# Performance work log

Hardware: AMD Instinct MI355X
Metric: run time of the kernel (lower is better)

Reference implementation:

```python
import jax, jax.numpy as jnp
import numpy as np

EPS = 1e-5

def bn_eval(x, p):
    # p: [4, C] = gamma, beta, running_mean, running_var; channel-last broadcast
    g, b, m, v = p[0], p[1], p[2], p[3]
    return (x - m) * (g / jnp.sqrt(v + EPS)) + b

def _bn_params(k, c):
    k1, k2, k3, k4 = jax.random.split(k, 4)
    gamma = jax.random.uniform(k1, (c,)) + 0.5
    beta = jax.random.normal(k2, (c,)) * 0.1
    mean = jax.random.normal(k3, (c,)) * 0.1
    var = jax.random.uniform(k4, (c,)) + 0.5
    return jnp.stack([gamma, beta, mean, var])

def _lin(k, fan_in, fan_out):
    bound = 1.0 / np.sqrt(fan_in)
    kw, kb = jax.random.split(k)
    w = jax.random.uniform(kw, (fan_in, fan_out), minval=-bound, maxval=bound)
    b = jax.random.uniform(kb, (fan_out,), minval=-bound, maxval=bound)
    return w, b

def setup_inputs() -> dict:
    key = jax.random.key(0)
    B, N, S, C, G = 2, 4096, 16, 256, 8
    ks = jax.random.split(key, 20)
    feats = jax.random.normal(ks[0], (B, N, C), dtype=jnp.float32)
    coords = jax.random.normal(ks[1], (B, N, 3), dtype=jnp.float32)
    index = jax.random.randint(ks[2], (B, N, S), 0, N, dtype=jnp.int32)
    wq, bq = _lin(ks[3], C, C); bnq = _bn_params(ks[4], C)
    wk, bk = _lin(ks[5], C, C); bnk = _bn_params(ks[6], C)
    wv, bv = _lin(ks[7], C, C)
    pm_w1, pm_b1 = _lin(ks[8], 3, C); pm_bn = _bn_params(ks[9], C)
    pm_w2, pm_b2 = _lin(ks[10], C, C)
    pb_w1, pb_b1 = _lin(ks[11], 3, C); pb_bn = _bn_params(ks[12], C)
    pb_w2, pb_b2 = _lin(ks[13], C, C)
    we_w1, we_b1 = _lin(ks[14], C, G); we_bn = _bn_params(ks[15], G)
    we_w2, we_b2 = _lin(ks[16], G, G)
    return dict(feats=feats, coords=coords, index=index,
                wq=wq, bq=bq, bnq=bnq, wk=wk, bk=bk, bnk=bnk, wv=wv, bv=bv,
                pm_w1=pm_w1, pm_b1=pm_b1, pm_bn=pm_bn, pm_w2=pm_w2, pm_b2=pm_b2,
                pb_w1=pb_w1, pb_b1=pb_b1, pb_bn=pb_bn, pb_w2=pb_w2, pb_b2=pb_b2,
                we_w1=we_w1, we_b1=we_b1, we_bn=we_bn, we_w2=we_w2, we_b2=we_b2)

def reference(feats, coords, index,
              wq, bq, bnq, wk, bk, bnk, wv, bv,
              pm_w1, pm_b1, pm_bn, pm_w2, pm_b2,
              pb_w1, pb_b1, pb_bn, pb_w2, pb_b2,
              we_w1, we_b1, we_bn, we_w2, we_b2):
    B, N, C = feats.shape
    S = index.shape[2]
    G = we_w1.shape[1]
    q = jax.nn.relu(bn_eval(feats @ wq + bq, bnq))                       # [B,N,C]
    k = jax.nn.relu(bn_eval(feats @ wk + bk, bnk))                       # [B,N,C]
    v = feats @ wv + bv                                                   # [B,N,C]
    idx = index.reshape(B, N * S)
    key_g = jnp.take_along_axis(k, idx[:, :, None], axis=1).reshape(B, N, S, C)
    val_g = jnp.take_along_axis(v, idx[:, :, None], axis=1).reshape(B, N, S, C)
    crd_g = jnp.take_along_axis(coords, idx[:, :, None], axis=1).reshape(B, N, S, 3)
    relation_qk = key_g - q[:, :, None, :]                                # [B,N,S,C]
    pos = coords[:, :, None, :] - crd_g                                   # [B,N,S,3]
    pem = jax.nn.relu(bn_eval(pos @ pm_w1 + pm_b1, pm_bn)) @ pm_w2 + pm_b2
    relation_qk = relation_qk * pem
    peb = jax.nn.relu(bn_eval(pos @ pb_w1 + pb_b1, pb_bn)) @ pb_w2 + pb_b2
    relation_qk = relation_qk + peb
    val_g = val_g + peb
    w = jax.nn.relu(bn_eval(relation_qk @ we_w1 + we_b1, we_bn)) @ we_w2 + we_b2  # [B,N,S,G]
    w = jax.nn.softmax(w, axis=2)                                         # softmax over neighbors
    val_g = val_g.reshape(B, N, S, G, C // G)
    out = jnp.einsum('bnsgi,bnsg->bngi', val_g, w).reshape(B, N, C)
    return out
```

## Files before the change

kernel.cpp:

```cpp
#include <hip/hip_runtime.h>
#include <hip/hip_bf16.h>


typedef __attribute__((ext_vector_type(8))) short bf16x8_t;
typedef __attribute__((ext_vector_type(4))) float f32x4_t;

#define BN_EPS 1e-5f
#define WSYNC() asm volatile("s_waitcnt lgkmcnt(0)" ::: "memory")

__device__ __forceinline__ float blo(unsigned int v) {
    union { unsigned int u; float f; } x; x.u = v << 16; return x.f;
}
__device__ __forceinline__ float bhi(unsigned int v) {
    union { unsigned int u; float f; } x; x.u = v & 0xffff0000u; return x.f;
}
__device__ __forceinline__ unsigned int fbits(float f) {
    union { float f; unsigned int u; } x; x.f = f; return x.u;
}
__device__ __forceinline__ unsigned short f2b(float f) {
    unsigned int u = fbits(f);
    return (unsigned short)((u + 0x7fffu + ((u >> 16) & 1u)) >> 16);
}
__device__ __forceinline__ unsigned int f2bpk(float a, float b) {
    union { __hip_bfloat162 h; unsigned int u; } x;
    x.h = __float22bfloat162_rn(make_float2(a, b));
    return x.u;
}
__device__ __forceinline__ unsigned int relpair(unsigned int kb, unsigned int qb,
                                                unsigned int pm_, unsigned int pb_) {
    float r0 = (blo(kb) - blo(qb)) * blo(pm_) + blo(pb_);
    float r1 = (bhi(kb) - bhi(qb)) * bhi(pm_) + bhi(pb_);
    return f2bpk(r0, r1);
}

__global__ __launch_bounds__(256) void k_prep(
    const float* __restrict__ wq, const float* __restrict__ wk,
    const float* __restrict__ wv, const float* __restrict__ pm2,
    const float* __restrict__ pb2,
    const float* __restrict__ pm_w1, const float* __restrict__ pm_b1,
    const float* __restrict__ pm_bn,
    const float* __restrict__ pb_w1, const float* __restrict__ pb_b1,
    const float* __restrict__ pb_bn,
    const float* __restrict__ we_w1,
    unsigned short* __restrict__ wsT, float* __restrict__ W4,
    unsigned short* __restrict__ we1TF)
{
    const int bid = blockIdx.x, t = threadIdx.x;
    if (bid < 160) {
        __shared__ unsigned short T[32][72];
        const int mat = bid >> 5;
        const int kk  = (bid >> 2) & 7;
        const int ntq = bid & 3;
        const float* s = (mat == 0) ? wq : (mat == 1) ? wk : (mat == 2) ? wv
                         : (mat == 3) ? pm2 : pb2;
        {
            int c = t & 63, r0 = t >> 6;
            for (int i = 0; i < 8; ++i) {
                int r = r0 + i * 4;
                T[r][c] = f2b(s[(kk * 32 + r) * 256 + ntq * 64 + c]);
            }
        }
        __syncthreads();
        {
            int seg = t >> 6, lane = t & 63;
            int col = seg * 16 + (lane & 15);
            int kr  = (lane >> 4) * 8;
            unsigned int v[8];
            #pragma unroll
            for (int j = 0; j < 8; ++j) v[j] = T[kr + j][col];
            uint4 o;
            o.x = v[0] | (v[1] << 16);
            o.y = v[2] | (v[3] << 16);
            o.z = v[4] | (v[5] << 16);
            o.w = v[6] | (v[7] << 16);
            *(uint4*)(wsT + mat * 65536 + (ntq * 4 + seg) * 4096 + kk * 512 + lane * 8) = o;
        }
    } else if (bid == 160) {
        int c = t;
        float s = pm_bn[c] / sqrtf(pm_bn[768 + c] + BN_EPS);
        float4 wm = make_float4(pm_w1[c] * s, pm_w1[256 + c] * s, pm_w1[512 + c] * s,
                                (pm_b1[c] - pm_bn[512 + c]) * s + pm_bn[256 + c]);
        s = pb_bn[c] / sqrtf(pb_bn[768 + c] + BN_EPS);
        float4 wb = make_float4(pb_w1[c] * s, pb_w1[256 + c] * s, pb_w1[512 + c] * s,
                                (pb_b1[c] - pb_bn[512 + c]) * s + pb_bn[256 + c]);
        ((float4*)W4)[c]       = wm;
        ((float4*)W4)[256 + c] = wb;
    } else {
        for (int j = 0; j < 8; ++j) {
            int e = t * 8 + j;
            int g = e >> 8, c = e & 255;
            we1TF[g * 256 + c] = f2b(we_w1[c * 8 + g]);
        }
    }
}

__global__ __launch_bounds__(256) void k_qkv(
    const float* __restrict__ feats,
    const unsigned short* __restrict__ wT,
    const float* __restrict__ bq, const float* __restrict__ bnq,
    const float* __restrict__ bk, const float* __restrict__ bnk,
    const float* __restrict__ bv,
    unsigned short* __restrict__ qkv)
{
    __shared__ unsigned short A[32][264];
    const int t    = threadIdx.x;
    const int widx = blockIdx.x >> 8;
    const int mb   = blockIdx.x & 255;

    for (int i = 0; i < 8; ++i) {
        int row = 4 * i + (t >> 6), col = (t & 63) * 4;
        float4 f = *(const float4*)(feats + (mb * 32 + row) * 256 + col);
        *(uint2*)&A[row][col] = make_uint2(f2bpk(f.x, f.y), f2bpk(f.z, f.w));
    }
    __syncthreads();

    const int lane = t & 63, w = t >> 6;
    const int ln15 = lane & 15, quad = lane >> 4;
    const int mt = w & 1, nh = w >> 1;

    bf16x8_t afr[8];
    #pragma unroll
    for (int kk = 0; kk < 8; ++kk)
        afr[kk] = *(const bf16x8_t*)&A[mt * 16 + ln15][kk * 32 + quad * 8];

    const unsigned short* W = wT + widx * 65536;
    const float* bias = (widx == 0) ? bq : (widx == 1) ? bk : bv;
    const float* bn   = (widx == 0) ? bnq : (widx == 1) ? bnk : nullptr;
    unsigned short* dst = qkv + (size_t)widx * 8192 * 256;

    const f32x4_t fzero = {0.f, 0.f, 0.f, 0.f};
    f32x4_t acc[8];
    for (int j = 0; j < 8; ++j) acc[j] = fzero;

    #pragma unroll
    for (int kk = 0; kk < 8; ++kk) {
        #pragma unroll
        for (int j = 0; j < 8; ++j) {
            int nt = nh * 8 + j;
            bf16x8_t bfr = *(const bf16x8_t*)(W + ((nt * 8 + kk) * 64 + lane) * 8);
            acc[j] = __builtin_amdgcn_mfma_f32_16x16x32_bf16(afr[kk], bfr, acc[j], 0, 0, 0);
        }
    }

    float bb[8], sc[8], mu[8], be[8];
    #pragma unroll
    for (int j = 0; j < 8; ++j) {
        int c = (nh * 8 + j) * 16 + ln15;
        bb[j] = bias[c];
        if (bn) {
            sc[j] = bn[c] / sqrtf(bn[768 + c] + BN_EPS);
            be[j] = bn[256 + c];
            mu[j] = bn[512 + c];
        }
    }
    __syncthreads();
    #pragma unroll
    for (int j = 0; j < 8; ++j) {
        int c = (nh * 8 + j) * 16 + ln15;
        float y[4];
        for (int r = 0; r < 4; ++r) {
            y[r] = acc[j][r] + bb[j];
            if (bn) y[r] = fmaxf((y[r] - mu[j]) * sc[j] + be[j], 0.f);
        }
        for (int r = 0; r < 4; r += 2) {
            unsigned int pk = f2bpk(y[r], y[r + 1]);
            A[mt * 16 + quad * 4 + r][c]     = (unsigned short)pk;
            A[mt * 16 + quad * 4 + r + 1][c] = (unsigned short)(pk >> 16);
        }
    }
    __syncthreads();
    {
        int row = t >> 3, cc = (t & 7) * 32;
        #pragma unroll
        for (int j = 0; j < 4; ++j) {
            uint4 v = *(const uint4*)&A[row][cc + 8 * j];
            *(uint4*)(dst + (mb * 32 + row) * 256 + cc + 8 * j) = v;
        }
    }
}

__global__ __launch_bounds__(256, 2) void k_main(
    const float* __restrict__ coords,
    const int*   __restrict__ index,
    const unsigned short* __restrict__ qm,
    const unsigned short* __restrict__ km,
    const unsigned short* __restrict__ vm,
    const unsigned short* __restrict__ pmw2F,
    const unsigned short* __restrict__ pbw2F,
    const float* __restrict__ W4,
    const unsigned short* __restrict__ we1TF,
    const float* __restrict__ pm_b2, const float* __restrict__ pb_b2,
    const float* __restrict__ we_b1, const float* __restrict__ we_bn,
    const float* __restrict__ we_w2, const float* __restrict__ we_b2,
    float* __restrict__ out)
{
    __shared__ unsigned short bufR[64][264];
    __shared__ unsigned short bufP[64][264];
    __shared__ float posA[64][4];
    __shared__ float us_[64][8];
    __shared__ int   rowg_[64];
    __shared__ float we2s[8][8];
    __shared__ float web2[8];

    const int t  = threadIdx.x;
    const int P0 = blockIdx.x * 4;
    const int bb_ = P0 >> 12;
    const int w = t >> 6, lane = t & 63;
    const int ln15 = lane & 15, quad = lane >> 4;
    const int R0 = w * 16;
    const int Pg = P0 + w;

    const int rg = (bb_ << 12) + index[Pg * 16 + ln15];
    uint4 kpre[8];
    #pragma unroll
    for (int kk = 0; kk < 8; ++kk)
        kpre[kk] = *(const uint4*)(km + rg * 256 + kk * 32 + quad * 8);

    const int hc = lane * 4;
    float4 cm[4], cb[4];
    #pragma unroll
    for (int i = 0; i < 4; ++i) {
        cm[i] = ((const float4*)W4)[hc + i];
        cb[i] = ((const float4*)W4)[256 + hc + i];
    }
    float bb0[4], bb1[4];
    #pragma unroll
    for (int ntl = 0; ntl < 4; ++ntl) {
        int c = (w * 4 + ntl) * 16 + ln15;
        bb0[ntl] = pb_b2[c];
        bb1[ntl] = pm_b2[c];
    }

    const int g8 = ln15 & 7;
    const float swe_r = we_bn[g8] / sqrtf(we_bn[24 + g8] + BN_EPS);
    const float dwe_r = (we_b1[g8] - we_bn[16 + g8]) * swe_r + we_bn[8 + g8];

    if (lane < 16) {
        rowg_[R0 + lane] = rg;
        posA[R0 + lane][0] = coords[Pg * 3 + 0] - coords[rg * 3 + 0];
        posA[R0 + lane][1] = coords[Pg * 3 + 1] - coords[rg * 3 + 1];
        posA[R0 + lane][2] = coords[Pg * 3 + 2] - coords[rg * 3 + 2];
        posA[R0 + lane][3] = 0.f;
    }
    if (t < 64) we2s[t >> 3][t & 7] = we_w2[t];
    if (t < 8)  web2[t] = we_b2[t];
    WSYNC();

    #pragma unroll
    for (int m = 0; m < 16; ++m) {
        float4 p = *(const float4*)&posA[R0 + m][0];
        float h0 = fmaxf(p.x * cb[0].x + p.y * cb[0].y + p.z * cb[0].z + cb[0].w, 0.f);
        float h1 = fmaxf(p.x * cb[1].x + p.y * cb[1].y + p.z * cb[1].z + cb[1].w, 0.f);
        float h2 = fmaxf(p.x * cb[2].x + p.y * cb[2].y + p.z * cb[2].z + cb[2].w, 0.f);
        float h3 = fmaxf(p.x * cb[3].x + p.y * cb[3].y + p.z * cb[3].z + cb[3].w, 0.f);
        *(uint2*)&bufR[R0 + m][hc] = make_uint2(f2bpk(h0, h1), f2bpk(h2, h3));
    }
    __syncthreads();

    f32x4_t acc[4][4];
    #pragma unroll
    for (int a = 0; a < 4; ++a)
        for (int mt = 0; mt < 4; ++mt)
            acc[a][mt] = (f32x4_t){bb0[a], bb0[a], bb0[a], bb0[a]};
    #pragma unroll
    for (int kk = 0; kk < 8; ++kk) {
        bf16x8_t afr[4];
        #pragma unroll
        for (int mt = 0; mt < 4; ++mt)
            afr[mt] = *(const bf16x8_t*)&bufR[mt * 16 + ln15][kk * 32 + quad * 8];
        #pragma unroll
        for (int ntl = 0; ntl < 4; ++ntl) {
            int nt = w * 4 + ntl;
            bf16x8_t bfr = *(const bf16x8_t*)(pbw2F + ((nt * 8 + kk) * 64 + lane) * 8);
            #pragma unroll
            for (int mt = 0; mt < 4; ++mt)
                acc[ntl][mt] = __builtin_amdgcn_mfma_f32_16x16x32_bf16(afr[mt], bfr, acc[ntl][mt], 0, 0, 0);
        }
    }
    __syncthreads();

    #pragma unroll
    for (int ntl = 0; ntl < 4; ++ntl) {
        int c = (w * 4 + ntl) * 16 + ln15;
        for (int mt = 0; mt < 4; ++mt)
            for (int r = 0; r < 4; r += 2) {
                unsigned int pk = f2bpk(acc[ntl][mt][r], acc[ntl][mt][r + 1]);
                bufP[mt * 16 + quad * 4 + r][c]     = (unsigned short)pk;
                bufP[mt * 16 + quad * 4 + r + 1][c] = (unsigned short)(pk >> 16);
            }
    }
    #pragma unroll
    for (int m = 0; m < 16; ++m) {
        float4 p = *(const float4*)&posA[R0 + m][0];
        float h0 = fmaxf(p.x * cm[0].x + p.y * cm[0].y + p.z * cm[0].z + cm[0].w, 0.f);
        float h1 = fmaxf(p.x * cm[1].x + p.y * cm[1].y + p.z * cm[1].z + cm[1].w, 0.f);
        float h2 = fmaxf(p.x * cm[2].x + p.y * cm[2].y + p.z * cm[2].z + cm[2].w, 0.f);
        float h3 = fmaxf(p.x * cm[3].x + p.y * cm[3].y + p.z * cm[3].z + cm[3].w, 0.f);
        *(uint2*)&bufR[R0 + m][hc] = make_uint2(f2bpk(h0, h1), f2bpk(h2, h3));
    }
    __syncthreads();

    #pragma unroll
    for (int a = 0; a < 4; ++a)
        for (int mt = 0; mt < 4; ++mt)
            acc[a][mt] = (f32x4_t){bb1[a], bb1[a], bb1[a], bb1[a]};
    #pragma unroll
    for (int kk = 0; kk < 8; ++kk) {
        bf16x8_t afr[4];
        #pragma unroll
        for (int mt = 0; mt < 4; ++mt)
            afr[mt] = *(const bf16x8_t*)&bufR[mt * 16 + ln15][kk * 32 + quad * 8];
        #pragma unroll
        for (int ntl = 0; ntl < 4; ++ntl) {
            int nt = w * 4 + ntl;
            bf16x8_t bfr = *(const bf16x8_t*)(pmw2F + ((nt * 8 + kk) * 64 + lane) * 8);
            #pragma unroll
            for (int mt = 0; mt < 4; ++mt)
                acc[ntl][mt] = __builtin_amdgcn_mfma_f32_16x16x32_bf16(afr[mt], bfr, acc[ntl][mt], 0, 0, 0);
        }
    }
    __syncthreads();

    #pragma unroll
    for (int ntl = 0; ntl < 4; ++ntl) {
        int c = (w * 4 + ntl) * 16 + ln15;
        for (int mt = 0; mt < 4; ++mt)
            for (int r = 0; r < 4; r += 2) {
                unsigned int pk = f2bpk(acc[ntl][mt][r], acc[ntl][mt][r + 1]);
                bufR[mt * 16 + quad * 4 + r][c]     = (unsigned short)pk;
                bufR[mt * 16 + quad * 4 + r + 1][c] = (unsigned short)(pk >> 16);
            }
    }
    __syncthreads();

    {
        const bf16x8_t bz = {0, 0, 0, 0, 0, 0, 0, 0};
        f32x4_t lacc = {0.f, 0.f, 0.f, 0.f};
        #pragma unroll
        for (int kk = 0; kk < 8; ++kk) {
            int cb8 = kk * 32 + quad * 8;
            uint4 pm4 = *(const uint4*)&bufR[R0 + ln15][cb8];
            uint4 pb4 = *(const uint4*)&bufP[R0 + ln15][cb8];
            uint4 q4  = *(const uint4*)(qm + Pg * 256 + cb8);
            union { uint4 u; bf16x8_t v; } rr;
            rr.u.x = relpair(kpre[kk].x, q4.x, pm4.x, pb4.x);
            rr.u.y = relpair(kpre[kk].y, q4.y, pm4.y, pb4.y);
            rr.u.z = relpair(kpre[kk].z, q4.z, pm4.z, pb4.z);
            rr.u.w = relpair(kpre[kk].w, q4.w, pm4.w, pb4.w);
            bf16x8_t bfr = bz;
            if (ln15 < 8) bfr = *(const bf16x8_t*)(we1TF + ln15 * 256 + cb8);
            lacc = __builtin_amdgcn_mfma_f32_16x16x32_bf16(rr.v, bfr, lacc, 0, 0, 0);
        }
        if (ln15 < 8) {
            #pragma unroll
            for (int r = 0; r < 4; ++r)
                us_[R0 + quad * 4 + r][ln15] = fmaxf(lacc[r] * swe_r + dwe_r, 0.f);
        }
    }
    WSYNC();

    if (lane < 16) {
        float uv[8], l[8];
        #pragma unroll
        for (int gp = 0; gp < 8; ++gp) uv[gp] = us_[R0 + lane][gp];
        #pragma unroll
        for (int g = 0; g < 8; ++g) {
            float x = web2[g];
            for (int gp = 0; gp < 8; ++gp) x += uv[gp] * we2s[gp][g];
            l[g] = x;
        }
        #pragma unroll
        for (int g = 0; g < 8; ++g) us_[R0 + lane][g] = l[g];
    }
    WSYNC();

    if (lane < 8) {
        int g = lane;
        float mx = -1e30f;
        for (int s = 0; s < 16; ++s) mx = fmaxf(mx, us_[R0 + s][g]);
        float e[16], sum = 0.f;
        for (int s = 0; s < 16; ++s) { e[s] = __expf(us_[R0 + s][g] - mx); sum += e[s]; }
        float inv = 1.f / sum;
        for (int s = 0; s < 16; ++s) us_[R0 + s][g] = e[s] * inv;
    }
    WSYNC();

    {
        int c5 = lane * 4, g = lane >> 3;
        float a0 = 0.f, a1 = 0.f, a2 = 0.f, a3 = 0.f;
        #pragma unroll
        for (int s = 0; s < 16; ++s) {
            int rv = rowg_[R0 + s];
            float wv_ = us_[R0 + s][g];
            uint2 v4 = *(const uint2*)(vm + rv * 256 + c5);
            uint2 p4 = *(const uint2*)&bufP[R0 + s][c5];
            a0 += wv_ * (blo(v4.x) + blo(p4.x));
            a1 += wv_ * (bhi(v4.x) + bhi(p4.x));
            a2 += wv_ * (blo(v4.y) + blo(p4.y));
            a3 += wv_ * (bhi(v4.y) + bhi(p4.y));
        }
        *(float4*)(out + (size_t)Pg * 256 + c5) = make_float4(a0, a1, a2, a3);
    }
}

extern "C" void kernel_launch(void* const* d_in, const int* in_sizes, int n_in,
                              void* d_out, int out_size, void* d_ws, size_t ws_size,
                              hipStream_t stream)
{
    const float* feats  = (const float*)d_in[0];
    const float* coords = (const float*)d_in[1];
    const int*   index  = (const int*)d_in[2];
    const float* wq     = (const float*)d_in[3];
    const float* bq     = (const float*)d_in[4];
    const float* bnq    = (const float*)d_in[5];
    const float* wk     = (const float*)d_in[6];
    const float* bk     = (const float*)d_in[7];
    const float* bnk    = (const float*)d_in[8];
    const float* wv     = (const float*)d_in[9];
    const float* bv     = (const float*)d_in[10];
    const float* pm_w1  = (const float*)d_in[11];
    const float* pm_b1  = (const float*)d_in[12];
    const float* pm_bn  = (const float*)d_in[13];
    const float* pm_w2  = (const float*)d_in[14];
    const float* pm_b2  = (const float*)d_in[15];
    const float* pb_w1  = (const float*)d_in[16];
    const float* pb_b1  = (const float*)d_in[17];
    const float* pb_bn  = (const float*)d_in[18];
    const float* pb_w2  = (const float*)d_in[19];
    const float* pb_b2  = (const float*)d_in[20];
    const float* we_w1  = (const float*)d_in[21];
    const float* we_b1  = (const float*)d_in[22];
    const float* we_bn  = (const float*)d_in[23];
    const float* we_w2  = (const float*)d_in[24];
    const float* we_b2  = (const float*)d_in[25];

    unsigned short* qkv   = (unsigned short*)d_ws;
    unsigned short* wsT   = qkv + (size_t)3 * 8192 * 256;
    float*          W4    = (float*)(wsT + 5 * 65536);
    unsigned short* we1TF = (unsigned short*)(W4 + 2048);

    const size_t need = (size_t)13238272 + 8192 + 4096;
    if (ws_size < need) {
        hipMemsetAsync(d_out, 0, (size_t)out_size * 4, stream);
        return;
    }

    k_prep<<<162,  256, 0, stream>>>(wq, wk, wv, pm_w2, pb_w2,
                                     pm_w1, pm_b1, pm_bn,
                                     pb_w1, pb_b1, pb_bn,
                                     we_w1, wsT, W4, we1TF);
    k_qkv <<<768,  256, 0, stream>>>(feats, wsT, bq, bnq, bk, bnk, bv, qkv);
    k_main<<<2048, 256, 0, stream>>>(coords, index,
                                     qkv,
                                     qkv + (size_t)8192 * 256,
                                     qkv + (size_t)2 * 8192 * 256,
                                     wsT + 3 * 65536,
                                     wsT + 4 * 65536,
                                     W4, we1TF,
                                     pm_b2, pb_b2,
                                     we_b1, we_bn, we_w2, we_b2,
                                     (float*)d_out);
}
```

Measured before the change: 201.9 us.

## Split k_main work across 8 waves per block with partial we1 reductions

k_main now runs 512 threads per block: two waves share each point, each taking half the channel chunks for the positional MLP GEMMs, the we1 projection and the final weighted sum. The two partial we1 sums are combined through a new shared buffer after a block barrier, and the BN scale and shift are precomputed once into shared memory. Per-wave register load drops (fewer accumulators and prefetched keys), which is meant to raise occupancy and latency hiding. In exchange it adds block-wide __syncthreads, halves per-lane output vector width, and leaves half the waves idle during the softmax stages.

```diff
diff --git a/kernel.cpp b/kernel.cpp
--- a/kernel.cpp
+++ b/kernel.cpp
@@ -128,9 +128,8 @@
     const float* bn   = (widx == 0) ? bnq : (widx == 1) ? bnk : nullptr;
     unsigned short* dst = qkv + (size_t)widx * 8192 * 256;
 
-    const f32x4_t fzero = {0.f, 0.f, 0.f, 0.f};
     f32x4_t acc[8];
-    for (int j = 0; j < 8; ++j) acc[j] = fzero;
+    for (int j = 0; j < 8; ++j) acc[j] = (f32x4_t){0.f, 0.f, 0.f, 0.f};
 
     #pragma unroll
     for (int kk = 0; kk < 8; ++kk) {
@@ -179,7 +178,7 @@
     }
 }
 
-__global__ __launch_bounds__(256, 2) void k_main(
+__global__ __launch_bounds__(512, 4) void k_main(
     const float* __restrict__ coords,
     const int*   __restrict__ index,
     const unsigned short* __restrict__ qm,
@@ -197,71 +196,75 @@
     __shared__ unsigned short bufR[64][264];
     __shared__ unsigned short bufP[64][264];
     __shared__ float posA[64][4];
+    __shared__ float usP[2][64][8];
     __shared__ float us_[64][8];
     __shared__ int   rowg_[64];
     __shared__ float we2s[8][8];
-    __shared__ float web2[8];
-
-    const int t  = threadIdx.x;
-    const int P0 = blockIdx.x * 4;
+    __shared__ float web2[8], swe8[8], dwe8[8];
+
+    const int t   = threadIdx.x;
+    const int P0  = blockIdx.x * 4;
     const int bb_ = P0 >> 12;
     const int w = t >> 6, lane = t & 63;
     const int ln15 = lane & 15, quad = lane >> 4;
-    const int R0 = w * 16;
-    const int Pg = P0 + w;
+    const int p   = w >> 1, sub = w & 1;
+    const int R0  = p * 16;
+    const int Pg  = P0 + p;
 
     const int rg = (bb_ << 12) + index[Pg * 16 + ln15];
-    uint4 kpre[8];
-    #pragma unroll
-    for (int kk = 0; kk < 8; ++kk)
-        kpre[kk] = *(const uint4*)(km + rg * 256 + kk * 32 + quad * 8);
+    uint4 kpre[4];
+    #pragma unroll
+    for (int kk = 0; kk < 4; ++kk)
+        kpre[kk] = *(const uint4*)(km + rg * 256 + (sub * 4 + kk) * 32 + quad * 8);
+
+    if (lane < 8) {
+        int m  = w * 8 + lane;
+        int Pr = P0 + (m >> 4);
+        int rs = (bb_ << 12) + index[Pr * 16 + (m & 15)];
+        rowg_[m]   = rs;
+        posA[m][0] = coords[Pr * 3 + 0] - coords[rs * 3 + 0];
+        posA[m][1] = coords[Pr * 3 + 1] - coords[rs * 3 + 1];
+        posA[m][2] = coords[Pr * 3 + 2] - coords[rs * 3 + 2];
+        posA[m][3] = 0.f;
+    }
+    if (t < 64) we2s[t >> 3][t & 7] = we_w2[t];
+    if (t < 8) {
+        float s = we_bn[t] / sqrtf(we_bn[24 + t] + BN_EPS);
+        swe8[t] = s;
+        dwe8[t] = (we_b1[t] - we_bn[16 + t]) * s + we_bn[8 + t];
+        web2[t] = we_b2[t];
+    }
+    WSYNC();
 
     const int hc = lane * 4;
-    float4 cm[4], cb[4];
-    #pragma unroll
-    for (int i = 0; i < 4; ++i) {
-        cm[i] = ((const float4*)W4)[hc + i];
-        cb[i] = ((const float4*)W4)[256 + hc + i];
-    }
-    float bb0[4], bb1[4];
-    #pragma unroll
-    for (int ntl = 0; ntl < 4; ++ntl) {
-        int c = (w * 4 + ntl) * 16 + ln15;
-        bb0[ntl] = pb_b2[c];
-        bb1[ntl] = pm_b2[c];
-    }
-
-    const int g8 = ln15 & 7;
-    const float swe_r = we_bn[g8] / sqrtf(we_bn[24 + g8] + BN_EPS);
-    const float dwe_r = (we_b1[g8] - we_bn[16 + g8]) * swe_r + we_bn[8 + g8];
-
-    if (lane < 16) {
-        rowg_[R0 + lane] = rg;
-        posA[R0 + lane][0] = coords[Pg * 3 + 0] - coords[rg * 3 + 0];
-        posA[R0 + lane][1] = coords[Pg * 3 + 1] - coords[rg * 3 + 1];
-        posA[R0 + lane][2] = coords[Pg * 3 + 2] - coords[rg * 3 + 2];
-        posA[R0 + lane][3] = 0.f;
-    }
-    if (t < 64) we2s[t >> 3][t & 7] = we_w2[t];
-    if (t < 8)  web2[t] = we_b2[t];
-    WSYNC();
-
-    #pragma unroll
-    for (int m = 0; m < 16; ++m) {
-        float4 p = *(const float4*)&posA[R0 + m][0];
-        float h0 = fmaxf(p.x * cb[0].x + p.y * cb[0].y + p.z * cb[0].z + cb[0].w, 0.f);
-        float h1 = fmaxf(p.x * cb[1].x + p.y * cb[1].y + p.z * cb[1].z + cb[1].w, 0.f);
-        float h2 = fmaxf(p.x * cb[2].x + p.y * cb[2].y + p.z * cb[2].z + cb[2].w, 0.f);
-        float h3 = fmaxf(p.x * cb[3].x + p.y * cb[3].y + p.z * cb[3].z + cb[3].w, 0.f);
-        *(uint2*)&bufR[R0 + m][hc] = make_uint2(f2bpk(h0, h1), f2bpk(h2, h3));
-    }
-    __syncthreads();
-
-    f32x4_t acc[4][4];
-    #pragma unroll
-    for (int a = 0; a < 4; ++a)
-        for (int mt = 0; mt < 4; ++mt)
-            acc[a][mt] = (f32x4_t){bb0[a], bb0[a], bb0[a], bb0[a]};
+    const int hm = w * 8;
+
+    {
+        float4 c0 = ((const float4*)W4)[256 + hc];
+        float4 c1 = ((const float4*)W4)[256 + hc + 1];
+        float4 c2 = ((const float4*)W4)[256 + hc + 2];
+        float4 c3 = ((const float4*)W4)[256 + hc + 3];
+        #pragma unroll
+        for (int m = 0; m < 8; ++m) {
+            float4 pp = *(const float4*)&posA[hm + m][0];
+            float h0 = fmaxf(pp.x * c0.x + pp.y * c0.y + pp.z * c0.z + c0.w, 0.f);
+            float h1 = fmaxf(pp.x * c1.x + pp.y * c1.y + pp.z * c1.z + c1.w, 0.f);
+            float h2 = fmaxf(pp.x * c2.x + pp.y * c2.y + pp.z * c2.z + c2.w, 0.f);
+            float h3 = fmaxf(pp.x * c3.x + pp.y * c3.y + pp.z * c3.z + c3.w, 0.f);
+            *(uint2*)&bufR[hm + m][hc] = make_uint2(f2bpk(h0, h1), f2bpk(h2, h3));
+        }
+    }
+    __syncthreads();
+
+    f32x4_t acc[2][4];
+    {
+        float b0 = pb_b2[(w * 2    ) * 16 + ln15];
+        float b1 = pb_b2[(w * 2 + 1) * 16 + ln15];
+        for (int mt = 0; mt < 4; ++mt) {
+            acc[0][mt] = (f32x4_t){b0, b0, b0, b0};
+            acc[1][mt] = (f32x4_t){b1, b1, b1, b1};
+        }
+    }
     #pragma unroll
     for (int kk = 0; kk < 8; ++kk) {
         bf16x8_t afr[4];
@@ -269,8 +272,8 @@
         for (int mt = 0; mt < 4; ++mt)
             afr[mt] = *(const bf16x8_t*)&bufR[mt * 16 + ln15][kk * 32 + quad * 8];
         #pragma unroll
-        for (int ntl = 0; ntl < 4; ++ntl) {
-            int nt = w * 4 + ntl;
+        for (int ntl = 0; ntl < 2; ++ntl) {
+            int nt = w * 2 + ntl;
             bf16x8_t bfr = *(const bf16x8_t*)(pbw2F + ((nt * 8 + kk) * 64 + lane) * 8);
             #pragma unroll
             for (int mt = 0; mt < 4; ++mt)
@@ -280,8 +283,8 @@
     __syncthreads();
 
     #pragma unroll
-    for (int ntl = 0; ntl < 4; ++ntl) {
-        int c = (w * 4 + ntl) * 16 + ln15;
+    for (int ntl = 0; ntl < 2; ++ntl) {
+        int c = (w * 2 + ntl) * 16 + ln15;
         for (int mt = 0; mt < 4; ++mt)
             for (int r = 0; r < 4; r += 2) {
                 unsigned int pk = f2bpk(acc[ntl][mt][r], acc[ntl][mt][r + 1]);
@@ -289,21 +292,31 @@
                 bufP[mt * 16 + quad * 4 + r + 1][c] = (unsigned short)(pk >> 16);
             }
     }
-    #pragma unroll
-    for (int m = 0; m < 16; ++m) {
-        float4 p = *(const float4*)&posA[R0 + m][0];
-        float h0 = fmaxf(p.x * cm[0].x + p.y * cm[0].y + p.z * cm[0].z + cm[0].w, 0.f);
-        float h1 = fmaxf(p.x * cm[1].x + p.y * cm[1].y + p.z * cm[1].z + cm[1].w, 0.f);
-        float h2 = fmaxf(p.x * cm[2].x + p.y * cm[2].y + p.z * cm[2].z + cm[2].w, 0.f);
-        float h3 = fmaxf(p.x * cm[3].x + p.y * cm[3].y + p.z * cm[3].z + cm[3].w, 0.f);
-        *(uint2*)&bufR[R0 + m][hc] = make_uint2(f2bpk(h0, h1), f2bpk(h2, h3));
-    }
-    __syncthreads();
-
-    #pragma unroll
-    for (int a = 0; a < 4; ++a)
-        for (int mt = 0; mt < 4; ++mt)
-            acc[a][mt] = (f32x4_t){bb1[a], bb1[a], bb1[a], bb1[a]};
+    {
+        float4 c0 = ((const float4*)W4)[hc];
+        float4 c1 = ((const float4*)W4)[hc + 1];
+        float4 c2 = ((const float4*)W4)[hc + 2];
+        float4 c3 = ((const float4*)W4)[hc + 3];
+        #pragma unroll
+        for (int m = 0; m < 8; ++m) {
+            float4 pp = *(const float4*)&posA[hm + m][0];
+            float h0 = fmaxf(pp.x * c0.x + pp.y * c0.y + pp.z * c0.z + c0.w, 0.f);
+            float h1 = fmaxf(pp.x * c1.x + pp.y * c1.y + pp.z * c1.z + c1.w, 0.f);
+            float h2 = fmaxf(pp.x * c2.x + pp.y * c2.y + pp.z * c2.z + c2.w, 0.f);
+            float h3 = fmaxf(pp.x * c3.x + pp.y * c3.y + pp.z * c3.z + c3.w, 0.f);
+            *(uint2*)&bufR[hm + m][hc] = make_uint2(f2bpk(h0, h1), f2bpk(h2, h3));
+        }
+    }
+    __syncthreads();
+
+    {
+        float b0 = pm_b2[(w * 2    ) * 16 + ln15];
+        float b1 = pm_b2[(w * 2 + 1) * 16 + ln15];
+        for (int mt = 0; mt < 4; ++mt) {
+            acc[0][mt] = (f32x4_t){b0, b0, b0, b0};
+            acc[1][mt] = (f32x4_t){b1, b1, b1, b1};
+        }
+    }
     #pragma unroll
     for (int kk = 0; kk < 8; ++kk) {
         bf16x8_t afr[4];
@@ -311,8 +324,8 @@
         for (int mt = 0; mt < 4; ++mt)
             afr[mt] = *(const bf16x8_t*)&bufR[mt * 16 + ln15][kk * 32 + quad * 8];
         #pragma unroll
-        for (int ntl = 0; ntl < 4; ++ntl) {
-            int nt = w * 4 + ntl;
+        for (int ntl = 0; ntl < 2; ++ntl) {
+            int nt = w * 2 + ntl;
             bf16x8_t bfr = *(const bf16x8_t*)(pmw2F + ((nt * 8 + kk) * 64 + lane) * 8);
             #pragma unroll
             for (int mt = 0; mt < 4; ++mt)
@@ -322,8 +335,8 @@
     __syncthreads();
 
     #pragma unroll
-    for (int ntl = 0; ntl < 4; ++ntl) {
-        int c = (w * 4 + ntl) * 16 + ln15;
+    for (int ntl = 0; ntl < 2; ++ntl) {
+        int c = (w * 2 + ntl) * 16 + ln15;
         for (int mt = 0; mt < 4; ++mt)
             for (int r = 0; r < 4; r += 2) {
                 unsigned int pk = f2bpk(acc[ntl][mt][r], acc[ntl][mt][r + 1]);
@@ -337,8 +350,8 @@
         const bf16x8_t bz = {0, 0, 0, 0, 0, 0, 0, 0};
         f32x4_t lacc = {0.f, 0.f, 0.f, 0.f};
         #pragma unroll
-        for (int kk = 0; kk < 8; ++kk) {
-            int cb8 = kk * 32 + quad * 8;
+        for (int kk = 0; kk < 4; ++kk) {
+            int cb8 = (sub * 4 + kk) * 32 + quad * 8;
             uint4 pm4 = *(const uint4*)&bufR[R0 + ln15][cb8];
             uint4 pb4 = *(const uint4*)&bufP[R0 + ln15][cb8];
             uint4 q4  = *(const uint4*)(qm + Pg * 256 + cb8);
@@ -354,15 +367,19 @@
         if (ln15 < 8) {
             #pragma unroll
             for (int r = 0; r < 4; ++r)
-                us_[R0 + quad * 4 + r][ln15] = fmaxf(lacc[r] * swe_r + dwe_r, 0.f);
-        }
-    }
-    WSYNC();
-
-    if (lane < 16) {
+                usP[sub][R0 + quad * 4 + r][ln15] = lacc[r];
+        }
+    }
+    __syncthreads();
+
+    if (sub == 0 && lane < 16) {
+        int s = lane;
         float uv[8], l[8];
         #pragma unroll
-        for (int gp = 0; gp < 8; ++gp) uv[gp] = us_[R0 + lane][gp];
+        for (int g = 0; g < 8; ++g) {
+            float x = usP[0][R0 + s][g] + usP[1][R0 + s][g];
+            uv[g] = fmaxf(x * swe8[g] + dwe8[g], 0.f);
+        }
         #pragma unroll
         for (int g = 0; g < 8; ++g) {
             float x = web2[g];
@@ -370,11 +387,11 @@
             l[g] = x;
         }
         #pragma unroll
-        for (int g = 0; g < 8; ++g) us_[R0 + lane][g] = l[g];
+        for (int g = 0; g < 8; ++g) us_[R0 + s][g] = l[g];
     }
     WSYNC();
 
-    if (lane < 8) {
+    if (sub == 0 && lane < 8) {
         int g = lane;
         float mx = -1e30f;
         for (int s = 0; s < 16; ++s) mx = fmaxf(mx, us_[R0 + s][g]);
@@ -383,23 +400,22 @@
         float inv = 1.f / sum;
         for (int s = 0; s < 16; ++s) us_[R0 + s][g] = e[s] * inv;
     }
-    WSYNC();
-
-    {
-        int c5 = lane * 4, g = lane >> 3;
-        float a0 = 0.f, a1 = 0.f, a2 = 0.f, a3 = 0.f;
+    __syncthreads();
+
+    {
+        int idx2 = sub * 64 + lane;
+        int c5 = idx2 * 2, g = c5 >> 5;
+        float a0 = 0.f, a1 = 0.f;
         #pragma unroll
         for (int s = 0; s < 16; ++s) {
             int rv = rowg_[R0 + s];
             float wv_ = us_[R0 + s][g];
-            uint2 v4 = *(const uint2*)(vm + rv * 256 + c5);
-            uint2 p4 = *(const uint2*)&bufP[R0 + s][c5];
-            a0 += wv_ * (blo(v4.x) + blo(p4.x));
-            a1 += wv_ * (bhi(v4.x) + bhi(p4.x));
-            a2 += wv_ * (blo(v4.y) + blo(p4.y));
-            a3 += wv_ * (bhi(v4.y) + bhi(p4.y));
-        }
-        *(float4*)(out + (size_t)Pg * 256 + c5) = make_float4(a0, a1, a2, a3);
+            unsigned int v2 = *(const unsigned int*)(vm + rv * 256 + c5);
+            unsigned int p2 = *(const unsigned int*)&bufP[R0 + s][c5];
+            a0 += wv_ * (blo(v2) + blo(p2));
+            a1 += wv_ * (bhi(v2) + bhi(p2));
+        }
+        *(float2*)(out + (size_t)Pg * 256 + c5) = make_float2(a0, a1);
     }
 }
 
@@ -450,7 +466,7 @@
                                      pb_w1, pb_b1, pb_bn,
                                      we_w1, wsT, W4, we1TF);
     k_qkv <<<768,  256, 0, stream>>>(feats, wsT, bq, bnq, bk, bnk, bv, qkv);
-    k_main<<<2048, 256, 0, stream>>>(coords, index,
+    k_main<<<2048, 512, 0, stream>>>(coords, index,
                                      qkv,
                                      qkv + (size_t)8192 * 256,
                                      qkv + (size_t)2 * 8192 * 256,
```

Result: faster. 197.5 us (-2.2%).
